# Optimization experiments

Hardware: AMD Instinct MI355X
Metric: run time of the kernel (lower is better)

The kernel has to match this reference:

```python
import jax, jax.numpy as jnp
from jax import lax
import numpy as np

B, C, T = 512, 12, 4096
DS = 4          # int_downsize
STEPS = 7       # int_steps
KS = 51         # smooth_size
SIGMA = (KS - 1) // 2  # 25, per module: gaussian_filter1d(delta, smooth_centre)


def _gauss_kernel():
    # Replicates scipy.ndimage.gaussian_filter1d(delta, SIGMA) on a length-KS
    # delta array with default truncate=4.0 and mode='reflect'.
    r = int(4.0 * SIGMA + 0.5)
    x = np.arange(-r, r + 1)
    g = np.exp(-0.5 * (x / SIGMA) ** 2)
    g /= g.sum()
    delta = np.zeros(KS)
    delta[(KS - 1) // 2] = 1.0
    padded = np.pad(delta, r, mode='symmetric')  # scipy 'reflect' boundary
    filt = np.convolve(padded, g, mode='valid')  # len == KS (g is symmetric)
    return filt.astype(np.float32)


def resize_linear(x, factor):
    # F.interpolate(mode='linear', align_corners=False, recompute_scale_factor=False)
    Tin = x.shape[-1]
    Tout = int(Tin * factor)
    src = (jnp.arange(Tout, dtype=x.dtype) + 0.5) / factor - 0.5
    src = jnp.clip(src, 0.0, Tin - 1)
    i0 = jnp.floor(src).astype(jnp.int32)
    i1 = jnp.minimum(i0 + 1, Tin - 1)
    w = src - i0
    return x[..., i0] * (1.0 - w) + x[..., i1] * w


def resize_transform(x, factor):
    # ResizeTransformTime: resize the field AND rescale its magnitude
    if factor < 1:
        return factor * resize_linear(x, factor)
    elif factor > 1:
        return resize_linear(factor * x, factor)
    return x


def warp_1d(src, flow):
    # SpatialTransformer for 1D signals: torch fakes 2D grid_sample by repeating
    # src to [B,C,Tlen,2] and the grid to [B,1,Tlen,2]; with align_corners=True,
    # zeros padding, bilinear. The width-dim (size 2) interpolation collapses to a
    # scalar in-bounds weight xw since both width copies are identical.
    Tlen = src.shape[-1]
    new_locs = jnp.arange(Tlen, dtype=src.dtype) + flow          # [B,1,Tlen]
    v = 2.0 * (new_locs / (Tlen - 1) - 0.5)                      # normalized
    ix = (v + 1.0) * 0.5                                         # W=2 -> (W-1)=1
    iy = (v + 1.0) * 0.5 * (Tlen - 1)
    x0 = jnp.floor(ix)
    fx = ix - x0
    x0i = x0.astype(jnp.int32)
    xw = ((1.0 - fx) * ((x0i >= 0) & (x0i <= 1))
          + fx * ((x0i + 1 >= 0) & (x0i + 1 <= 1)))              # [B,1,Tlen]
    y0 = jnp.floor(iy)
    fy = iy - y0
    y0i = y0.astype(jnp.int32)
    y1i = y0i + 1
    vy0 = (y0i >= 0) & (y0i < Tlen)
    vy1 = (y1i >= 0) & (y1i < Tlen)
    y0c = jnp.clip(y0i, 0, Tlen - 1)
    y1c = jnp.clip(y1i, 0, Tlen - 1)
    Bc, Cc = src.shape[0], src.shape[1]
    idx0 = jnp.broadcast_to(y0c, (Bc, Cc, Tlen))
    idx1 = jnp.broadcast_to(y1c, (Bc, Cc, Tlen))
    g0 = jnp.take_along_axis(src, idx0, axis=-1)
    g1 = jnp.take_along_axis(src, idx1, axis=-1)
    return xw * ((1.0 - fy) * vy0 * g0 + fy * vy1 * g1)


def setup_inputs() -> dict:
    key = jax.random.key(0)
    k1, k2 = jax.random.split(key)
    source = jax.random.normal(k1, (B, C, T), dtype=jnp.float32)
    noise = jax.random.normal(k2, (B, 1, T), dtype=jnp.float32)
    flow_mag = jnp.ones((1,), dtype=jnp.float32)
    smooth_kernel = jnp.asarray(_gauss_kernel())
    return {"source": source, "flow_mag": flow_mag, "noise": noise,
            "smooth_kernel": smooth_kernel}


def reference(source, flow_mag, noise, smooth_kernel):
    flow_field = flow_mag * noise                      # [B,1,T]
    pos_flow = resize_transform(flow_field, 1.0 / DS)  # [B,1,T//DS]
    # VecInt: scaling and squaring
    vec = pos_flow * (1.0 / 2 ** STEPS)
    for _ in range(STEPS):
        vec = vec + warp_1d(vec, vec)
    pos_flow = resize_transform(vec, float(DS))        # back to [B,1,T]
    # conv1d smoothing (cross-correlation, same as F.conv1d)
    pad = (KS - 1) // 2
    pos_flow = lax.conv_general_dilated(
        pos_flow, smooth_kernel.reshape(1, 1, KS),
        window_strides=(1,), padding=[(pad, pad)],
        dimension_numbers=('NCH', 'OIH', 'NCH'))
    return warp_1d(source, pos_flow)
```

## Files before the change

### kernel.cpp

```cpp
#include <hip/hip_runtime.h>


#define BB 512
#define CC 12
#define TT 4096
#define TD 1024
#define KS 51
#define NT 1024
#define NJ 17
#define J0 (-8)
#define T_LO 32
#define T_HI 4063

typedef float f32x4 __attribute__((ext_vector_type(4)));
typedef float f32x2 __attribute__((ext_vector_type(2), aligned(4)));

struct WarpW { int y0c, y1c; float w0, w1; };
struct WarpP { int addr, o0, o1; float w0, w1; };

template <int TLEN>
__device__ __forceinline__ WarpW warp_weights(int t, float flow) {
    const float tm1 = (float)(TLEN - 1);
    float nl = (float)t + flow;
    float v  = 2.0f * (nl / tm1 - 0.5f);
    float ix = (v + 1.0f) * 0.5f;
    float iy = ix * tm1;
    float x0 = floorf(ix);
    float fx = ix - x0;
    int   x0i = (int)x0;
    float m0 = (x0i >= 0 && x0i <= 1) ? 1.0f : 0.0f;
    float m1 = (x0i + 1 >= 0 && x0i + 1 <= 1) ? 1.0f : 0.0f;
    float xw = (1.0f - fx) * m0 + fx * m1;
    float y0 = floorf(iy);
    float fy = iy - y0;
    int   y0i = (int)y0;
    int   y1i = y0i + 1;
    float vy0 = (y0i >= 0 && y0i < TLEN) ? 1.0f : 0.0f;
    float vy1 = (y1i >= 0 && y1i < TLEN) ? 1.0f : 0.0f;
    WarpW r;
    r.y0c = min(max(y0i, 0), TLEN - 1);
    r.y1c = min(max(y1i, 0), TLEN - 1);
    r.w0 = xw * (1.0f - fy) * vy0;
    r.w1 = xw * fy * vy1;
    return r;
}

template <int TLEN>
__device__ __forceinline__ WarpP warp_pack(int t, float flow) {
    const float tm1 = (float)(TLEN - 1);
    float nl = (float)t + flow;
    float v  = 2.0f * (nl / tm1 - 0.5f);
    float ix = (v + 1.0f) * 0.5f;
    float iy = ix * tm1;
    float x0 = floorf(ix);
    float fx = ix - x0;
    int   x0i = (int)x0;
    float m0 = (x0i >= 0 && x0i <= 1) ? 1.0f : 0.0f;
    float m1 = (x0i + 1 >= 0 && x0i + 1 <= 1) ? 1.0f : 0.0f;
    float xw = (1.0f - fx) * m0 + fx * m1;
    float y0 = floorf(iy);
    float fy = iy - y0;
    int   y0i = (int)y0;
    int   y1i = y0i + 1;
    float vy0 = (y0i >= 0 && y0i < TLEN) ? 1.0f : 0.0f;
    float vy1 = (y1i >= 0 && y1i < TLEN) ? 1.0f : 0.0f;
    int y0c = min(max(y0i, 0), TLEN - 1);
    int y1c = min(max(y1i, 0), TLEN - 1);
    WarpP r;
    r.addr = min(max(y0i, 0), TLEN - 2);
    r.o0   = y0c - r.addr;
    r.o1   = y1c - r.addr;
    r.w0   = xw * (1.0f - fy) * vy0;
    r.w1   = xw * fy * vy1;
    return r;
}

__device__ __forceinline__ float conv_direct(const float* __restrict__ vec,
                                             const float* __restrict__ g, int t) {
    float acc = 0.0f;
    for (int k = 0; k < KS; ++k) {
        int s = t + k - 25;
        if (s < 0 || s >= TT) continue;
        float srcp = 0.25f * (float)s - 0.375f;
        srcp = fminf(fmaxf(srcp, 0.0f), (float)(TD - 1));
        float flp = floorf(srcp);
        int i0 = (int)flp;
        int i1 = min(i0 + 1, TD - 1);
        float w = srcp - flp;
        acc += g[k] * 4.0f * ((1.0f - w) * vec[i0] + w * vec[i1]);
    }
    return acc;
}

extern "C" __global__ void __launch_bounds__(NT)
rand_warp_aug_kernel(const float* __restrict__ source,
                     const float* __restrict__ flow_mag,
                     const float* __restrict__ noise,
                     const float* __restrict__ gk,
                     float* __restrict__ out) {
    __shared__ float vecA[TD];
    __shared__ float vecB[TD];
    __shared__ float g[KS];
    __shared__ float wtab[NJ][4];

    const int b   = blockIdx.x;
    const int tid = threadIdx.x;
    const float fm = flow_mag[0];

    const f32x4* nrow4 = (const f32x4*)(noise + (size_t)b * TT);
    {
        f32x4 nv = nrow4[tid];
        float x1 = fm * nv.y;
        float x2 = fm * nv.z;
        vecA[tid] = (x1 * 0.5f + x2 * 0.5f) * (0.25f * 0.0078125f);
    }
    if (tid < KS) g[tid] = gk[tid];
    __syncthreads();

    if (tid < 4 * NJ) {
        int p = tid / NJ;
        int j = tid % NJ + J0;
        float acc = 0.0f;
        for (int k = 0; k < KS; ++k) {
            int q = p + k - 25;
            int d = (q >= 0) ? (q >> 2) : -((-q + 3) >> 2);
            int r = q - 4 * d;
            float c = 0.0f;
            if (r == 0)      { if (j == d - 1) c = 0.375f; else if (j == d) c = 0.625f; }
            else if (r == 1) { if (j == d - 1) c = 0.125f; else if (j == d) c = 0.875f; }
            else if (r == 2) { if (j == d)     c = 0.875f; else if (j == d + 1) c = 0.125f; }
            else             { if (j == d)     c = 0.625f; else if (j == d + 1) c = 0.375f; }
            acc += g[k] * c;
        }
        wtab[tid % NJ][p] = 4.0f * acc;
    }

    float* cur = vecA;
    float* nxt = vecB;
#pragma unroll 1
    for (int s = 0; s < 7; ++s) {
        {
            float fl = cur[tid];
            WarpW w = warp_weights<TD>(tid, fl);
            nxt[tid] = fl + (w.w0 * cur[w.y0c] + w.w1 * cur[w.y1c]);
        }
        __syncthreads();
        float* tmp = cur; cur = nxt; nxt = tmp;
    }

    const int p  = tid & 3;
    const int Tb = tid >> 2;
    float pf[4];
    {
        float a0 = 0.0f, a1 = 0.0f, a2 = 0.0f, a3 = 0.0f;
#pragma unroll
        for (int j = 0; j < NJ; ++j) {
            float wreg = wtab[j][p];
            int base = Tb + j + J0;
            a0 += wreg * cur[base];
            a1 += wreg * cur[base + 256];
            a2 += wreg * cur[base + 512];
            a3 += wreg * cur[base + 768];
        }
        pf[0] = a0; pf[1] = a1; pf[2] = a2; pf[3] = a3;
    }
    if (tid < T_LO)                  pf[0] = conv_direct(cur, g, tid);
    if (tid >= NT - (TT - 1 - T_HI)) pf[3] = conv_direct(cur, g, tid + 3 * NT);

    const float* sbase = source + (size_t)b * CC * TT;
    float*       obase = out    + (size_t)b * CC * TT;
#pragma unroll
    for (int tt = 0; tt < TT / NT; ++tt) {
        int t = tid + tt * NT;
        WarpP w = warp_pack<TT>(t, pf[tt]);
#pragma unroll
        for (int c = 0; c < CC; ++c) {
            const float* srow = sbase + (size_t)c * TT;
            f32x2 v = *(const f32x2*)(srow + w.addr);
            float g0 = w.o0 ? v.y : v.x;
            float g1 = w.o1 ? v.y : v.x;
            float o = w.w0 * g0 + w.w1 * g1;
            __builtin_nontemporal_store(o, obase + (size_t)c * TT + t);
        }
    }
}

extern "C" void kernel_launch(void* const* d_in, const int* in_sizes, int n_in,
                              void* d_out, int out_size, void* d_ws, size_t ws_size,
                              hipStream_t stream) {
    const float* source   = (const float*)d_in[0];
    const float* flow_mag = (const float*)d_in[1];
    const float* noise    = (const float*)d_in[2];
    const float* gk       = (const float*)d_in[3];
    float* out = (float*)d_out;

    rand_warp_aug_kernel<<<BB, NT, 0, stream>>>(source, flow_mag, noise, gk, out);
}
```

Baseline: 54.23 us.

## Stage source rows in LDS with vectorized loads before warp gather

```diff
diff --git a/kernel.cpp b/kernel.cpp
--- a/kernel.cpp
+++ b/kernel.cpp
@@ -13,10 +13,9 @@
 #define T_HI 4063
 
 typedef float f32x4 __attribute__((ext_vector_type(4)));
-typedef float f32x2 __attribute__((ext_vector_type(2), aligned(4)));
 
 struct WarpW { int y0c, y1c; float w0, w1; };
-struct WarpP { int addr, o0, o1; float w0, w1; };
+struct WarpG { int addr; float a, b; };
 
 template <int TLEN>
 __device__ __forceinline__ WarpW warp_weights(int t, float flow) {
@@ -46,7 +45,7 @@
 }
 
 template <int TLEN>
-__device__ __forceinline__ WarpP warp_pack(int t, float flow) {
+__device__ __forceinline__ WarpG warp_gather(int t, float flow) {
     const float tm1 = (float)(TLEN - 1);
     float nl = (float)t + flow;
     float v  = 2.0f * (nl / tm1 - 0.5f);
@@ -66,12 +65,14 @@
     float vy1 = (y1i >= 0 && y1i < TLEN) ? 1.0f : 0.0f;
     int y0c = min(max(y0i, 0), TLEN - 1);
     int y1c = min(max(y1i, 0), TLEN - 1);
-    WarpP r;
+    float w0 = xw * (1.0f - fy) * vy0;
+    float w1 = xw * fy * vy1;
+    WarpG r;
     r.addr = min(max(y0i, 0), TLEN - 2);
-    r.o0   = y0c - r.addr;
-    r.o1   = y1c - r.addr;
-    r.w0   = xw * (1.0f - fy) * vy0;
-    r.w1   = xw * fy * vy1;
+    int o0 = y0c - r.addr;
+    int o1 = y1c - r.addr;
+    r.a = (o0 ? 0.0f : w0) + (o1 ? 0.0f : w1);
+    r.b = (o0 ? w0 : 0.0f) + (o1 ? w1 : 0.0f);
     return r;
 }
 
@@ -100,6 +101,7 @@
                      float* __restrict__ out) {
     __shared__ float vecA[TD];
     __shared__ float vecB[TD];
+    __shared__ float buf[TT];
     __shared__ float g[KS];
     __shared__ float wtab[NJ][4];
 
@@ -167,20 +169,27 @@
     if (tid < T_LO)                  pf[0] = conv_direct(cur, g, tid);
     if (tid >= NT - (TT - 1 - T_HI)) pf[3] = conv_direct(cur, g, tid + 3 * NT);
 
-    const float* sbase = source + (size_t)b * CC * TT;
-    float*       obase = out    + (size_t)b * CC * TT;
+    WarpG wg[4];
 #pragma unroll
-    for (int tt = 0; tt < TT / NT; ++tt) {
-        int t = tid + tt * NT;
-        WarpP w = warp_pack<TT>(t, pf[tt]);
+    for (int tt = 0; tt < 4; ++tt)
+        wg[tt] = warp_gather<TT>(tid + tt * NT, pf[tt]);
+
+    const f32x4* sbase4 = (const f32x4*)(source + (size_t)b * CC * TT);
+    float*       obase  = out + (size_t)b * CC * TT;
+    f32x4 r = sbase4[tid];
+#pragma unroll 1
+    for (int c = 0; c < CC; ++c) {
+        __syncthreads();
+        ((f32x4*)buf)[tid] = r;
+        if (c + 1 < CC) r = sbase4[(size_t)(c + 1) * (TT / 4) + tid];
+        __syncthreads();
+        float* orow = obase + (size_t)c * TT;
 #pragma unroll
-        for (int c = 0; c < CC; ++c) {
-            const float* srow = sbase + (size_t)c * TT;
-            f32x2 v = *(const f32x2*)(srow + w.addr);
-            float g0 = w.o0 ? v.y : v.x;
-            float g1 = w.o1 ? v.y : v.x;
-            float o = w.w0 * g0 + w.w1 * g1;
-            __builtin_nontemporal_store(o, obase + (size_t)c * TT + t);
+        for (int tt = 0; tt < 4; ++tt) {
+            int t = tid + tt * NT;
+            float v0 = buf[wg[tt].addr];
+            float v1 = buf[wg[tt].addr + 1];
+            __builtin_nontemporal_store(wg[tt].a * v0 + wg[tt].b * v1, orow + t);
         }
     }
 }
```

After: 58.31 us. 7.5% more time.
